# Optimization experiments

Hardware: AMD Instinct MI355X
Metric: run time of the kernel (lower is better)

Reference implementation:

```python
import jax, jax.numpy as jnp
import numpy as np

B, N, D_IN, D_OUT = 4, 4096, 512, 512

def setup_inputs() -> dict:
    key = jax.random.key(0)
    k1, k2, k3, k4 = jax.random.split(key, 4)
    x = jax.random.normal(k1, (B, N, D_IN), dtype=jnp.float32)
    A_shape = jax.random.uniform(k2, (B, N, N), dtype=jnp.float32)
    w = jax.random.normal(k3, (D_IN, D_OUT), dtype=jnp.float32)
    a = jax.random.normal(k4, (D_OUT,), dtype=jnp.float32)
    return {"x": x, "A_shape": A_shape, "w": w, "a": a}

def reference(x, A_shape, w, a):
    # y = x @ w ; pairwise score A[i,j] = (y_i + y_j) @ a = s_i + s_j
    y = x @ w                                  # [B, N, D_out]
    s = y @ a                                  # [B, N]
    A = s[..., :, None] + s[..., None, :]      # [B, N, N] (== (x1+x2) @ a)
    A = jnp.tanh(A / 8.0) * 8.0                # soft clip to (-8, 8)
    A = jnp.where(A >= 0, A, 0.1 * A)          # LeakyReLU(0.1)
    A = jnp.exp(A) * A_shape                   # masked exp
    A = A / jnp.sum(A, axis=-1, keepdims=True) # row-normalize
    A = A * jnp.sum(A_shape, axis=-1, keepdims=True)  # rescale by degree
    out = (A @ x) @ w                          # aggregate then project: [B, N, D_out]
    return out
```

## Files before the change

### kernel.cpp

```cpp
#include <hip/hip_runtime.h>
#include <hip/hip_bf16.h>


typedef __attribute__((ext_vector_type(4))) float f32x4;
typedef __attribute__((ext_vector_type(8))) short short8;

#define NN 4096
#define DD 512
#define BN_TOT 16384

__device__ __forceinline__ short f2bf(float f) {
    union { float f; unsigned u; } x;
    x.f = f;
    unsigned r = x.u + 0x7FFFu + ((x.u >> 16) & 1u);
    return (short)(r >> 16);
}

__device__ __forceinline__ float gfun(float t) {
    float e = __expf(t * 0.25f);
    float c = 8.0f - 16.0f * __builtin_amdgcn_rcpf(e + 1.0f);
    c = (c >= 0.0f) ? c : 0.1f * c;
    return __expf(c);
}

__global__ __launch_bounds__(256) void k_wt(const float* __restrict__ w,
                                            short* __restrict__ wT) {
    int tid = blockIdx.x * 256 + threadIdx.x;
    int d = tid >> 9, k = tid & 511;
    wT[tid] = f2bf(w[(size_t)k * 512 + d]);
}

__global__ __launch_bounds__(256) void k_v(const float* __restrict__ w,
                                           const float* __restrict__ a,
                                           float* __restrict__ v) {
    int gw = (blockIdx.x * 256 + threadIdx.x) >> 6;
    int l = threadIdx.x & 63;
    const float* row = w + (size_t)gw * 512 + l * 8;
    const float* ap = a + l * 8;
    float4 w0 = *(const float4*)(row);
    float4 w1 = *(const float4*)(row + 4);
    float4 a0 = *(const float4*)(ap);
    float4 a1 = *(const float4*)(ap + 4);
    float p = w0.x * a0.x + w0.y * a0.y + w0.z * a0.z + w0.w * a0.w +
              w1.x * a1.x + w1.y * a1.y + w1.z * a1.z + w1.w * a1.w;
#pragma unroll
    for (int off = 32; off > 0; off >>= 1) p += __shfl_down(p, off);
    if (l == 0) v[gw] = p;
}

__global__ __launch_bounds__(256) void k_s_x16(const float* __restrict__ x,
                                               const float* __restrict__ v,
                                               float* __restrict__ s,
                                               short* __restrict__ x16) {
    __shared__ float vs[512];
    int t = threadIdx.x;
    vs[t] = v[t];
    vs[t + 256] = v[t + 256];
    __syncthreads();
    int w = t >> 6, l = t & 63;
    size_t row = (size_t)blockIdx.x * 4 + w;
    const float* xr = x + row * 512 + l * 8;
    float4 x0 = *(const float4*)(xr);
    float4 x1 = *(const float4*)(xr + 4);
    const float* vp = vs + l * 8;
    float p = x0.x * vp[0] + x0.y * vp[1] + x0.z * vp[2] + x0.w * vp[3] +
              x1.x * vp[4] + x1.y * vp[5] + x1.z * vp[6] + x1.w * vp[7];
    short8 pk;
    pk[0] = f2bf(x0.x); pk[1] = f2bf(x0.y); pk[2] = f2bf(x0.z); pk[3] = f2bf(x0.w);
    pk[4] = f2bf(x1.x); pk[5] = f2bf(x1.y); pk[6] = f2bf(x1.z); pk[7] = f2bf(x1.w);
    *(short8*)(x16 + row * 512 + l * 8) = pk;
#pragma unroll
    for (int off = 32; off > 0; off >>= 1) p += __shfl_down(p, off);
    if (l == 0) s[row] = p;
}

__global__ __launch_bounds__(256, 2) void k_ygemm(const short* __restrict__ wT,
                                                  const short* __restrict__ x16,
                                                  short* __restrict__ yT) {
    __shared__ __align__(16) short At[128 * 72];
    __shared__ __align__(16) short Bt[128 * 72];
    const int t = threadIdx.x;
    const int w = t >> 6, l = t & 63;
    const int mt = blockIdx.x & 3, nt = blockIdx.x >> 2;
    const int wr = w >> 1, wc = w & 1;
    f32x4 acc[4][4];
#pragma unroll
    for (int i = 0; i < 4; ++i)
#pragma unroll
        for (int j = 0; j < 4; ++j) acc[i][j] = (f32x4){0.f, 0.f, 0.f, 0.f};

    const short* Ag = wT + (size_t)(mt * 128 + (t >> 3)) * 512 + (t & 7) * 8;
    const short* Bg = x16 + (size_t)(nt * 128 + (t >> 3)) * 512 + (t & 7) * 8;
    short* Aw = At + (t >> 3) * 72 + (t & 7) * 8;
    short* Bw = Bt + (t >> 3) * 72 + (t & 7) * 8;
    const short* Ar = At + (wr * 64 + (l & 15)) * 72 + (l >> 4) * 8;
    const short* Br = Bt + (wc * 64 + (l & 15)) * 72 + (l >> 4) * 8;

    short8 va[4], vb[4];
#pragma unroll
    for (int ii = 0; ii < 4; ++ii) {
        va[ii] = *(const short8*)(Ag + (size_t)ii * 32 * 512);
        vb[ii] = *(const short8*)(Bg + (size_t)ii * 32 * 512);
    }

    for (int kk = 0; kk < 8; ++kk) {
        __syncthreads();
#pragma unroll
        for (int ii = 0; ii < 4; ++ii) {
            *(short8*)(Aw + ii * 32 * 72) = va[ii];
            *(short8*)(Bw + ii * 32 * 72) = vb[ii];
        }
        __syncthreads();
        if (kk < 7) {
            const int k0 = (kk + 1) * 64;
#pragma unroll
            for (int ii = 0; ii < 4; ++ii) {
                va[ii] = *(const short8*)(Ag + (size_t)ii * 32 * 512 + k0);
                vb[ii] = *(const short8*)(Bg + (size_t)ii * 32 * 512 + k0);
            }
        }
#pragma unroll
        for (int ks = 0; ks < 2; ++ks) {
            short8 af[4], bfr[4];
#pragma unroll
            for (int it = 0; it < 4; ++it)
                af[it] = *(const short8*)(Ar + it * 16 * 72 + ks * 32);
#pragma unroll
            for (int jt = 0; jt < 4; ++jt)
                bfr[jt] = *(const short8*)(Br + jt * 16 * 72 + ks * 32);
#pragma unroll
            for (int it = 0; it < 4; ++it)
#pragma unroll
                for (int jt = 0; jt < 4; ++jt)
                    acc[it][jt] = __builtin_amdgcn_mfma_f32_16x16x32_bf16(
                        af[it], bfr[jt], acc[it][jt], 0, 0, 0);
        }
    }
#pragma unroll
    for (int it = 0; it < 4; ++it)
#pragma unroll
        for (int jt = 0; jt < 4; ++jt)
#pragma unroll
            for (int r = 0; r < 4; ++r) {
                int drow = mt * 128 + wr * 64 + it * 16 + (l >> 4) * 4 + r;
                int bn = nt * 128 + wc * 64 + jt * 16 + (l & 15);
                yT[(size_t)drow * BN_TOT + bn] = f2bf(acc[it][jt][r]);
            }
}

__global__ __launch_bounds__(256, 2) void k_fused(const float* __restrict__ mask,
                                                  const float* __restrict__ s,
                                                  const short* __restrict__ yT,
                                                  float* __restrict__ out) {
    __shared__ __align__(16) short P[2][32 * 72];
    __shared__ float scl[32];
    const int t = threadIdx.x;
    const int w = t >> 6, l = t & 63;
    const int b = blockIdx.x >> 7;
    const int i0 = (blockIdx.x & 127) << 5;
    const int i = t >> 3;
    const int seg = t & 7;
    const float s_i = s[b * NN + i0 + i];
    const float* mrow = mask + (size_t)(b * NN + i0 + i) * NN + seg * 8;
    const float* sb = s + b * NN + seg * 8;
    const short* ybase = yT + (size_t)(w * 128 + (l & 15)) * BN_TOT + b * NN + ((l >> 4) * 8);
    const int pwoff = i * 72 + seg * 8;
    const int proff = (l & 15) * 72 + (l >> 4) * 8;

    f32x4 acc[2][8];
#pragma unroll
    for (int a1 = 0; a1 < 2; ++a1)
#pragma unroll
        for (int a2 = 0; a2 < 8; ++a2) acc[a1][a2] = (f32x4){0.f, 0.f, 0.f, 0.f};
    float r_part = 0.f, deg_part = 0.f;

    float4 m0 = *(const float4*)(mrow);
    float4 m1 = *(const float4*)(mrow + 4);
    float4 sj0 = *(const float4*)(sb);
    float4 sj1 = *(const float4*)(sb + 4);

    for (int jt = 0; jt < 64; ++jt) {
        const int buf = jt & 1;
        float mv[8] = {m0.x, m0.y, m0.z, m0.w, m1.x, m1.y, m1.z, m1.w};
        float sv[8] = {sj0.x, sj0.y, sj0.z, sj0.w, sj1.x, sj1.y, sj1.z, sj1.w};

        short8 bfr[16];
        const short* yb = ybase + jt * 64;
#pragma unroll
        for (int ks = 0; ks < 2; ++ks)
#pragma unroll
            for (int dt = 0; dt < 8; ++dt)
                bfr[ks * 8 + dt] =
                    *(const short8*)(yb + (size_t)dt * 16 * BN_TOT + ks * 32);

        if (jt < 63) {
            const int j0n = (jt + 1) * 64;
            m0 = *(const float4*)(mrow + j0n);
            m1 = *(const float4*)(mrow + j0n + 4);
            sj0 = *(const float4*)(sb + j0n);
            sj1 = *(const float4*)(sb + j0n + 4);
        }

        short8 pk;
#pragma unroll
        for (int e = 0; e < 8; ++e) {
            float p = gfun(s_i + sv[e]) * mv[e];
            deg_part += mv[e];
            r_part += p;
            pk[e] = f2bf(p);
        }
        *(short8*)(P[buf] + pwoff) = pk;

        __syncthreads();

#pragma unroll
        for (int ks = 0; ks < 2; ++ks) {
            short8 a0 = *(const short8*)(P[buf] + proff + ks * 32);
            short8 a1 = *(const short8*)(P[buf] + proff + 16 * 72 + ks * 32);
#pragma unroll
            for (int dt = 0; dt < 8; ++dt) {
                acc[0][dt] = __builtin_amdgcn_mfma_f32_16x16x32_bf16(
                    a0, bfr[ks * 8 + dt], acc[0][dt], 0, 0, 0);
                acc[1][dt] = __builtin_amdgcn_mfma_f32_16x16x32_bf16(
                    a1, bfr[ks * 8 + dt], acc[1][dt], 0, 0, 0);
            }
        }
    }
#pragma unroll
    for (int off = 1; off < 8; off <<= 1) {
        r_part += __shfl_xor(r_part, off);
        deg_part += __shfl_xor(deg_part, off);
    }
    if (seg == 0) scl[i] = deg_part / r_part;
    __syncthreads();
#pragma unroll
    for (int it = 0; it < 2; ++it)
#pragma unroll
        for (int r = 0; r < 4; ++r) {
            const int row = it * 16 + (l >> 4) * 4 + r;
            const float sc = scl[row];
            float* op = out + (size_t)(b * NN + i0 + row) * 512 + w * 128 + (l & 15);
#pragma unroll
            for (int dt = 0; dt < 8; ++dt) op[dt * 16] = acc[it][dt][r] * sc;
        }
}

extern "C" void kernel_launch(void* const* d_in, const int* in_sizes, int n_in,
                              void* d_out, int out_size, void* d_ws, size_t ws_size,
                              hipStream_t stream) {
    const float* x = (const float*)d_in[0];
    const float* mask = (const float*)d_in[1];
    const float* w = (const float*)d_in[2];
    const float* a = (const float*)d_in[3];
    float* out = (float*)d_out;
    char* ws = (char*)d_ws;
    short* wT = (short*)(ws);
    float* v = (float*)(ws + 524288);
    float* s = (float*)(ws + 526336);
    short* x16 = (short*)(ws + 591872);
    short* yT = (short*)(ws + 17369088);

    hipLaunchKernelGGL(k_wt, dim3(1024), dim3(256), 0, stream, w, wT);
    hipLaunchKernelGGL(k_v, dim3(128), dim3(256), 0, stream, w, a, v);
    hipLaunchKernelGGL(k_s_x16, dim3(4096), dim3(256), 0, stream, x, v, s, x16);
    hipLaunchKernelGGL(k_ygemm, dim3(512), dim3(256), 0, stream, wT, x16, yT);
    hipLaunchKernelGGL(k_fused, dim3(512), dim3(256), 0, stream, mask, s, yT, out);
}
```

Measured before the change: 584.6 us.

## Split fused attention-aggregate across 8 waves per block and interleave batches

The fused mask/exp/aggregate kernel now runs 512 threads per block. Each of the 8 waves owns 64 output columns instead of 128, and each thread computes 4 mask elements instead of 8. Blocks are remapped so neighbouring block IDs cover different batches, mask loads and output stores use nontemporal hints, and __syncthreads is replaced with a raw lgkmcnt wait plus s_barrier. This raises occupancy and halves per-thread registers, but every wave now re-reads the P tile from LDS and the y fragments are loaded by more waves in total.

```diff
diff --git a/kernel.cpp b/kernel.cpp
--- a/kernel.cpp
+++ b/kernel.cpp
@@ -4,10 +4,13 @@
 
 typedef __attribute__((ext_vector_type(4))) float f32x4;
 typedef __attribute__((ext_vector_type(8))) short short8;
+typedef __attribute__((ext_vector_type(4))) short s16x4;
 
 #define NN 4096
 #define DD 512
 #define BN_TOT 16384
+
+#define LDS_BARRIER() __asm__ __volatile__("s_waitcnt lgkmcnt(0)\n\ts_barrier" ::: "memory")
 
 __device__ __forceinline__ short f2bf(float f) {
     union { float f; unsigned u; } x;
@@ -19,7 +22,7 @@
 __device__ __forceinline__ float gfun(float t) {
     float e = __expf(t * 0.25f);
     float c = 8.0f - 16.0f * __builtin_amdgcn_rcpf(e + 1.0f);
-    c = (c >= 0.0f) ? c : 0.1f * c;
+    c = fmaxf(c, 0.1f * c);
     return __expf(c);
 }
 
@@ -37,10 +40,10 @@
     int l = threadIdx.x & 63;
     const float* row = w + (size_t)gw * 512 + l * 8;
     const float* ap = a + l * 8;
-    float4 w0 = *(const float4*)(row);
-    float4 w1 = *(const float4*)(row + 4);
-    float4 a0 = *(const float4*)(ap);
-    float4 a1 = *(const float4*)(ap + 4);
+    f32x4 w0 = *(const f32x4*)(row);
+    f32x4 w1 = *(const f32x4*)(row + 4);
+    f32x4 a0 = *(const f32x4*)(ap);
+    f32x4 a1 = *(const f32x4*)(ap + 4);
     float p = w0.x * a0.x + w0.y * a0.y + w0.z * a0.z + w0.w * a0.w +
               w1.x * a1.x + w1.y * a1.y + w1.z * a1.z + w1.w * a1.w;
 #pragma unroll
@@ -60,8 +63,8 @@
     int w = t >> 6, l = t & 63;
     size_t row = (size_t)blockIdx.x * 4 + w;
     const float* xr = x + row * 512 + l * 8;
-    float4 x0 = *(const float4*)(xr);
-    float4 x1 = *(const float4*)(xr + 4);
+    f32x4 x0 = *(const f32x4*)(xr);
+    f32x4 x1 = *(const f32x4*)(xr + 4);
     const float* vp = vs + l * 8;
     float p = x0.x * vp[0] + x0.y * vp[1] + x0.z * vp[2] + x0.w * vp[3] +
               x1.x * vp[4] + x1.y * vp[5] + x1.z * vp[6] + x1.w * vp[7];
@@ -104,13 +107,13 @@
     }
 
     for (int kk = 0; kk < 8; ++kk) {
-        __syncthreads();
+        LDS_BARRIER();
 #pragma unroll
         for (int ii = 0; ii < 4; ++ii) {
             *(short8*)(Aw + ii * 32 * 72) = va[ii];
             *(short8*)(Bw + ii * 32 * 72) = vb[ii];
         }
-        __syncthreads();
+        LDS_BARRIER();
         if (kk < 7) {
             const int k0 = (kk + 1) * 64;
 #pragma unroll
@@ -148,7 +151,7 @@
             }
 }
 
-__global__ __launch_bounds__(256, 2) void k_fused(const float* __restrict__ mask,
+__global__ __launch_bounds__(512, 4) void k_fused(const float* __restrict__ mask,
                                                   const float* __restrict__ s,
                                                   const short* __restrict__ yT,
                                                   float* __restrict__ out) {
@@ -156,78 +159,77 @@
     __shared__ float scl[32];
     const int t = threadIdx.x;
     const int w = t >> 6, l = t & 63;
-    const int b = blockIdx.x >> 7;
-    const int i0 = (blockIdx.x & 127) << 5;
-    const int i = t >> 3;
-    const int seg = t & 7;
+    const int bx = blockIdx.x;
+    const int b = (bx & 7) >> 1;
+    const int u = ((bx >> 3) << 1) | (bx & 1);
+    const int i0 = u << 5;
+    const int i = t >> 4;
+    const int seg = t & 15;
     const float s_i = s[b * NN + i0 + i];
-    const float* mrow = mask + (size_t)(b * NN + i0 + i) * NN + seg * 8;
-    const float* sb = s + b * NN + seg * 8;
-    const short* ybase = yT + (size_t)(w * 128 + (l & 15)) * BN_TOT + b * NN + ((l >> 4) * 8);
-    const int pwoff = i * 72 + seg * 8;
+    const float* mrow = mask + (size_t)(b * NN + i0 + i) * NN + seg * 4;
+    const float* sb = s + b * NN + seg * 4;
+    const int d0 = w * 64;
+    const short* ybase = yT + (size_t)(d0 + (l & 15)) * BN_TOT + b * NN + ((l >> 4) * 8);
+    const int pwoff = i * 72 + seg * 4;
     const int proff = (l & 15) * 72 + (l >> 4) * 8;
 
-    f32x4 acc[2][8];
+    f32x4 acc[2][4];
 #pragma unroll
     for (int a1 = 0; a1 < 2; ++a1)
 #pragma unroll
-        for (int a2 = 0; a2 < 8; ++a2) acc[a1][a2] = (f32x4){0.f, 0.f, 0.f, 0.f};
+        for (int a2 = 0; a2 < 4; ++a2) acc[a1][a2] = (f32x4){0.f, 0.f, 0.f, 0.f};
     float r_part = 0.f, deg_part = 0.f;
 
-    float4 m0 = *(const float4*)(mrow);
-    float4 m1 = *(const float4*)(mrow + 4);
-    float4 sj0 = *(const float4*)(sb);
-    float4 sj1 = *(const float4*)(sb + 4);
+    f32x4 m0 = __builtin_nontemporal_load((const f32x4*)(mrow));
+    f32x4 sj = *(const f32x4*)(sb);
 
     for (int jt = 0; jt < 64; ++jt) {
         const int buf = jt & 1;
-        float mv[8] = {m0.x, m0.y, m0.z, m0.w, m1.x, m1.y, m1.z, m1.w};
-        float sv[8] = {sj0.x, sj0.y, sj0.z, sj0.w, sj1.x, sj1.y, sj1.z, sj1.w};
-
-        short8 bfr[16];
+        float mv[4] = {m0.x, m0.y, m0.z, m0.w};
+        float sv[4] = {sj.x, sj.y, sj.z, sj.w};
+
+        short8 bfr[8];
         const short* yb = ybase + jt * 64;
 #pragma unroll
         for (int ks = 0; ks < 2; ++ks)
 #pragma unroll
-            for (int dt = 0; dt < 8; ++dt)
-                bfr[ks * 8 + dt] =
+            for (int dt = 0; dt < 4; ++dt)
+                bfr[ks * 4 + dt] =
                     *(const short8*)(yb + (size_t)dt * 16 * BN_TOT + ks * 32);
 
         if (jt < 63) {
             const int j0n = (jt + 1) * 64;
-            m0 = *(const float4*)(mrow + j0n);
-            m1 = *(const float4*)(mrow + j0n + 4);
-            sj0 = *(const float4*)(sb + j0n);
-            sj1 = *(const float4*)(sb + j0n + 4);
-        }
-
-        short8 pk;
-#pragma unroll
-        for (int e = 0; e < 8; ++e) {
+            m0 = __builtin_nontemporal_load((const f32x4*)(mrow + j0n));
+            sj = *(const f32x4*)(sb + j0n);
+        }
+
+        s16x4 pk;
+#pragma unroll
+        for (int e = 0; e < 4; ++e) {
             float p = gfun(s_i + sv[e]) * mv[e];
             deg_part += mv[e];
             r_part += p;
             pk[e] = f2bf(p);
         }
-        *(short8*)(P[buf] + pwoff) = pk;
-
-        __syncthreads();
+        *(s16x4*)(P[buf] + pwoff) = pk;
+
+        LDS_BARRIER();
 
 #pragma unroll
         for (int ks = 0; ks < 2; ++ks) {
             short8 a0 = *(const short8*)(P[buf] + proff + ks * 32);
             short8 a1 = *(const short8*)(P[buf] + proff + 16 * 72 + ks * 32);
 #pragma unroll
-            for (int dt = 0; dt < 8; ++dt) {
+            for (int dt = 0; dt < 4; ++dt) {
                 acc[0][dt] = __builtin_amdgcn_mfma_f32_16x16x32_bf16(
-                    a0, bfr[ks * 8 + dt], acc[0][dt], 0, 0, 0);
+                    a0, bfr[ks * 4 + dt], acc[0][dt], 0, 0, 0);
                 acc[1][dt] = __builtin_amdgcn_mfma_f32_16x16x32_bf16(
-                    a1, bfr[ks * 8 + dt], acc[1][dt], 0, 0, 0);
+                    a1, bfr[ks * 4 + dt], acc[1][dt], 0, 0, 0);
             }
         }
     }
 #pragma unroll
-    for (int off = 1; off < 8; off <<= 1) {
+    for (int off = 1; off < 16; off <<= 1) {
         r_part += __shfl_xor(r_part, off);
         deg_part += __shfl_xor(deg_part, off);
     }
@@ -239,9 +241,10 @@
         for (int r = 0; r < 4; ++r) {
             const int row = it * 16 + (l >> 4) * 4 + r;
             const float sc = scl[row];
-            float* op = out + (size_t)(b * NN + i0 + row) * 512 + w * 128 + (l & 15);
-#pragma unroll
-            for (int dt = 0; dt < 8; ++dt) op[dt * 16] = acc[it][dt][r] * sc;
+            float* op = out + (size_t)(b * NN + i0 + row) * 512 + d0 + (l & 15);
+#pragma unroll
+            for (int dt = 0; dt < 4; ++dt)
+                __builtin_nontemporal_store(acc[it][dt][r] * sc, op + dt * 16);
         }
 }
 
@@ -264,5 +267,5 @@
     hipLaunchKernelGGL(k_v, dim3(128), dim3(256), 0, stream, w, a, v);
     hipLaunchKernelGGL(k_s_x16, dim3(4096), dim3(256), 0, stream, x, v, s, x16);
     hipLaunchKernelGGL(k_ygemm, dim3(512), dim3(256), 0, stream, wT, x16, yT);
-    hipLaunchKernelGGL(k_fused, dim3(512), dim3(256), 0, stream, mask, s, yT, out);
-}
+    hipLaunchKernelGGL(k_fused, dim3(512), dim3(512), 0, stream, mask, s, yT, out);
+}
```

Result: no change. 590.6 us (+1.0%).
